# Kernel tuning notes

Measured on AMD Instinct MI355X. Metric: run time of the kernel, lower is better.

The kernel has to match this reference:

```python
import jax, jax.numpy as jnp
import numpy as np
from jax.scipy.special import logsumexp

K, D, H, A = 8, 512, 512, 1024
S, T = 64, 128
B = S * T


def setup_inputs() -> dict:
    key = jax.random.key(0)
    k1, k2, k3, k4 = jax.random.split(key, 4)
    obs = jax.random.normal(k1, (B, D), dtype=jnp.float32)
    actions = jax.random.randint(k2, (B,), 0, A, dtype=jnp.int64)
    # uniform mixture prior (log(1/K)) => all components supported
    start_mixture_logprobs = jnp.full((S, K), jnp.log(1.0 / K), dtype=jnp.float32)
    W1 = jax.random.normal(k3, (K, D, H), dtype=jnp.float32) * 0.02
    b1 = jnp.zeros((K, H), dtype=jnp.float32)
    W2 = jax.random.normal(k4, (K, H, A), dtype=jnp.float32) * 0.02
    b2 = jnp.zeros((K, A), dtype=jnp.float32)
    return {"obs": obs, "actions": actions,
            "start_mixture_logprobs": start_mixture_logprobs,
            "W1": W1, "b1": b1, "W2": W2, "b2": b2, "seq_len": T}


def reference(obs, actions, start_mixture_logprobs, W1, b1, W2, b2, seq_len):
    num_seqs, num_comp = start_mixture_logprobs.shape
    batch = obs.shape[0]
    t_len = batch // num_seqs  # == seq_len
    num_out = W2.shape[-1]

    # per-component MLP on the full batch (all components supported)
    h = jax.nn.relu(jnp.einsum('bd,kdh->kbh', obs, W1) + b1[:, None, :])
    logits = jnp.einsum('kbh,kha->kba', h, W2) + b2[:, None, :]  # [K,B,A]
    component_logprobs = jax.nn.log_softmax(logits, axis=2)      # [K,B,A]

    # add time dimension: [B, K, A] -> [S, T, K, A]
    clp_t = component_logprobs.transpose(1, 0, 2).reshape(num_seqs, t_len, num_comp, num_out)
    act_t = actions.reshape(num_seqs, t_len)

    # gather logprob of taken action per component: [S, T, K]
    idx = jnp.broadcast_to(act_t[:, :, None, None], (num_seqs, t_len, num_comp, 1))
    action_logprobs = jnp.take_along_axis(clp_t, idx, axis=3)[..., 0]
    cum = jnp.cumsum(action_logprobs, axis=1)  # [S,T,K]

    # per-timestep posterior over mixture (shifted cumulative evidence)
    shift = jnp.concatenate([jnp.zeros((num_seqs, 1, num_comp), dtype=cum.dtype), cum[:, :-1]], axis=1)
    mix = jax.nn.log_softmax(start_mixture_logprobs[:, None, :] + shift, axis=2)  # [S,T,K]
    final_mixture_logprobs = jax.nn.log_softmax(start_mixture_logprobs + cum[:, -1], axis=1)

    # combine: logsumexp over components of component_logprobs + mixture logprob
    mix_flat = mix.reshape(batch, num_comp).T  # [K,B]
    model_out = logsumexp(component_logprobs + mix_flat[:, :, None], axis=0)  # [B,A]
    return model_out, final_mixture_logprobs
```

## Files before the change

### kernel.cpp

```cpp
#include <hip/hip_runtime.h>
#include <hip/hip_bf16.h>
#include <stdint.h>

#define KC   8
#define DIM  512
#define HID  512
#define ACTN 1024
#define NS   64
#define NT   128
#define NB   8192
#define PB   8

typedef __attribute__((ext_vector_type(8))) short short8;
typedef __attribute__((ext_vector_type(8))) unsigned short ushort8;
typedef __attribute__((ext_vector_type(4))) float floatx4;

__device__ inline float bf2f(unsigned short u) {
    return __uint_as_float(((unsigned int)u) << 16);
}
__device__ inline unsigned short f2bf(float x) {
    return __builtin_bit_cast(unsigned short, __float2bfloat16(x));
}

__device__ inline void gload_lds16(const unsigned short* g, unsigned short* l) {
    __builtin_amdgcn_global_load_lds(
        (const __attribute__((address_space(1))) unsigned int*)g,
        (__attribute__((address_space(3))) unsigned int*)l,
        16, 0, 0);
}

__global__ __launch_bounds__(256) void obs_blk_kernel(
    const float* __restrict__ in, unsigned short* __restrict__ out)
{
    int mg = blockIdx.x;
#pragma unroll
    for (int rep = 0; rep < 16; ++rep) {
        int idx = rep * 256 + threadIdx.x;
        int kc  = idx >> 6;
        int row = idx & 63;
        const float* p = in + ((size_t)(mg * 64 + row) * DIM) + kc * 8;
        ushort8 u;
#pragma unroll
        for (int e = 0; e < 8; e++) u[e] = f2bf(p[e]);
        *(ushort8*)(out + (((size_t)mg * (DIM / 8) + kc) << 9) + (row << 3)) = u;
    }
}

__global__ __launch_bounds__(256) void wblk_kernel(
    const float* __restrict__ in, unsigned short* __restrict__ out, int R, int C)
{
    __shared__ float tile[64][65];
    int z = blockIdx.z;
    const float* src = in + (size_t)z * R * C;
    unsigned short* dst = out + (size_t)z * R * C;
    int h0 = blockIdx.x * 64, d0 = blockIdx.y * 64;
    int tx = threadIdx.x & 63, ty = threadIdx.x >> 6;
#pragma unroll
    for (int i = 0; i < 64; i += 4)
        tile[ty + i][tx] = src[(size_t)(d0 + ty + i) * C + h0 + tx];
    __syncthreads();
    int KCHR = R >> 3;
#pragma unroll
    for (int rep = 0; rep < 2; ++rep) {
        int idx  = rep * 256 + threadIdx.x;
        int h_l  = idx & 63;
        int dc_l = idx >> 6;
        ushort8 u;
#pragma unroll
        for (int e = 0; e < 8; e++) u[e] = f2bf(tile[dc_l * 8 + e][h_l]);
        size_t off = ((((size_t)(h0 >> 6) * KCHR) + (d0 >> 3) + dc_l) << 9) + (h_l << 3);
        *(ushort8*)(dst + off) = u;
    }
}

__global__ __launch_bounds__(256, 4) void gemm_blk_kernel(
    const unsigned short* __restrict__ Aall,
    const unsigned short* __restrict__ Ball,
    const float* __restrict__ biasall,
    unsigned short* __restrict__ Call,
    const int* __restrict__ actions,
    float* __restrict__ pmax, float* __restrict__ psum, float* __restrict__ palp,
    int M, int N, int Kd,
    long long zsA, long long zsB,
    int strideBias, long long strideC,
    int do_relu, int do_lse, int do_blocked)
{
    __shared__ __align__(16) unsigned short S[17408];
    unsigned short* const As = S;
    unsigned short* const Bs = S + 4096;

    const int zb = blockIdx.z;
    const float* bias = biasall + (size_t)zb * strideBias;
    unsigned short* Cb = Call + (size_t)zb * strideC;

    const int tid  = threadIdx.x;
    const int lane = tid & 63;
    const int wave = tid >> 6;
    const int wm = wave >> 1;
    const int wn = wave & 1;
    const int quad = lane >> 4;
    const int l16  = lane & 15;

    const int bm = blockIdx.x * 128;
    const int bn = blockIdx.y * 128;
    const int KCH = Kd >> 3;

    floatx4 acc[4][4];
#pragma unroll
    for (int i = 0; i < 4; i++)
#pragma unroll
        for (int j = 0; j < 4; j++)
            acc[i][j] = (floatx4){0.f, 0.f, 0.f, 0.f};

    const int loff = lane << 3;
    const unsigned short* pA = Aall + (size_t)zb * zsA + (((size_t)(bm >> 6) * KCH + wave) << 9) + loff;
    const unsigned short* pB = Ball + (size_t)zb * zsB + (((size_t)(bn >> 6) * KCH + wave) << 9) + loff;
    const size_t mgs = (size_t)KCH << 9;
    unsigned short* ldsA = As + wave * 1024;
    unsigned short* ldsB = Bs + wave * 1024;

    const int nk = Kd >> 5;
    for (int it = 0; it < nk; ++it) {
        __syncthreads();
        gload_lds16(pA,       ldsA);
        gload_lds16(pA + mgs, ldsA + 512);
        gload_lds16(pB,       ldsB);
        gload_lds16(pB + mgs, ldsB + 512);
        pA += 2048; pB += 2048;
        __syncthreads();

        short8 af[4], bfr[4];
#pragma unroll
        for (int i = 0; i < 4; i++)
            af[i] = *(const short8*)(As + quad * 1024 + ((wm * 64 + i * 16 + l16) << 3));
#pragma unroll
        for (int j = 0; j < 4; j++)
            bfr[j] = *(const short8*)(Bs + quad * 1024 + ((wn * 64 + j * 16 + l16) << 3));
#pragma unroll
        for (int i = 0; i < 4; i++)
#pragma unroll
            for (int j = 0; j < 4; j++)
                acc[i][j] = __builtin_amdgcn_mfma_f32_16x16x32_bf16(
                    af[i], bfr[j], acc[i][j], 0, 0, 0);
    }
    __syncthreads();

    unsigned short* const Cs = S;
#pragma unroll
    for (int j = 0; j < 4; j++) {
        int col = wn * 64 + j * 16 + l16;
        float bv = bias[bn + col];
#pragma unroll
        for (int i = 0; i < 4; i++) {
            int rw = wm * 64 + i * 16 + quad * 4;
#pragma unroll
            for (int r = 0; r < 4; r++) {
                float v = acc[i][j][r] + bv;
                if (do_relu) v = fmaxf(v, 0.f);
                Cs[(rw + r) * 136 + col] = f2bf(v);
            }
        }
    }
    __syncthreads();

    if (do_blocked) {
        const int KCHo = N >> 3;
#pragma unroll
        for (int rep = 0; rep < 8; ++rep) {
            int idx  = rep * 256 + tid;
            int kc_l = idx >> 7;
            int row  = idx & 127;
            ushort8 u = *(const ushort8*)&Cs[row * 136 + kc_l * 8];
            size_t off = ((((size_t)((bm >> 6) + (row >> 6)) * KCHo) + (bn >> 3) + kc_l) << 9)
                       + ((row & 63) << 3);
            *(ushort8*)(Cb + off) = u;
        }
    } else {
        const int row = tid >> 1;
        const int ch  = (tid & 1) * 64;

        float allm = 0.f;
        if (do_lse) {
            float m = -1e30f;
#pragma unroll
            for (int j = 0; j < 8; j++) {
                ushort8 u = *(const ushort8*)&Cs[row * 136 + ch + 8 * j];
#pragma unroll
                for (int e = 0; e < 8; e++) m = fmaxf(m, bf2f(u[e]));
            }
            allm = fmaxf(m, __shfl_xor(m, 1));
        }

        unsigned short* crow = Cb + (size_t)(bm + row) * N + bn + ch;
        float s = 0.f;
#pragma unroll
        for (int j = 0; j < 8; j++) {
            ushort8 u = *(const ushort8*)&Cs[row * 136 + ch + 8 * j];
            *(ushort8*)(crow + 8 * j) = u;
            if (do_lse) {
#pragma unroll
                for (int e = 0; e < 8; e++) s += __expf(bf2f(u[e]) - allm);
            }
        }

        if (do_lse) {
            float stot = s + __shfl_xor(s, 1);
            size_t kb = (size_t)zb * M + bm + row;
            if ((tid & 1) == 0) {
                pmax[kb * PB + blockIdx.y] = allm;
                psum[kb * PB + blockIdx.y] = stot;
            }
            int act = actions[bm + row];
            int rel = act - bn - ch;
            if (rel >= 0 && rel < 64)
                palp[kb] = bf2f(Cs[row * 136 + act - bn]);
        }
    }
}

__global__ __launch_bounds__(256) void lse_finish_kernel(
    const float* __restrict__ pmax, const float* __restrict__ psum,
    const float* __restrict__ palp,
    float* __restrict__ lse, float* __restrict__ alp)
{
    int kb = blockIdx.x * 256 + threadIdx.x;
    float m[PB];
#pragma unroll
    for (int p = 0; p < PB; p++) m[p] = pmax[(size_t)kb * PB + p];
    float M = m[0];
#pragma unroll
    for (int p = 1; p < PB; p++) M = fmaxf(M, m[p]);
    float S = 0.f;
#pragma unroll
    for (int p = 0; p < PB; p++) S += psum[(size_t)kb * PB + p] * __expf(m[p] - M);
    float l = M + __logf(S);
    lse[kb] = l;
    alp[kb] = palp[kb] - l;
}

__global__ __launch_bounds__(128) void mix_kernel(
    const float* __restrict__ alp,
    const float* __restrict__ start,
    const float* __restrict__ lse,
    float* __restrict__ w,
    float* __restrict__ fmix)
{
    __shared__ float buf[2][NT][9];
    int s = blockIdx.x, t = threadIdx.x;
    int b = s * NT + t;
    float a[KC];
#pragma unroll
    for (int k = 0; k < KC; k++) a[k] = alp[(size_t)k * NB + b];
#pragma unroll
    for (int k = 0; k < KC; k++) buf[0][t][k] = a[k];
    int p = 0;
    for (int off = 1; off < NT; off <<= 1) {
        __syncthreads();
#pragma unroll
        for (int k = 0; k < KC; k++) {
            float x = buf[p][t][k];
            if (t >= off) x += buf[p][t - off][k];
            buf[1 - p][t][k] = x;
        }
        p ^= 1;
    }
    __syncthreads();
    float st[KC], e[KC];
#pragma unroll
    for (int k = 0; k < KC; k++) st[k] = start[s * KC + k];
#pragma unroll
    for (int k = 0; k < KC; k++) e[k] = st[k] + buf[p][t][k] - a[k];
    float m = e[0];
#pragma unroll
    for (int k = 1; k < KC; k++) m = fmaxf(m, e[k]);
    float sum = 0.f;
#pragma unroll
    for (int k = 0; k < KC; k++) sum += __expf(e[k] - m);
    float l = m + __logf(sum);
#pragma unroll
    for (int k = 0; k < KC; k++)
        w[(size_t)k * NB + b] = (e[k] - l) - lse[(size_t)k * NB + b];

    if (t == NT - 1) {
        float f[KC];
#pragma unroll
        for (int k = 0; k < KC; k++) f[k] = st[k] + buf[p][t][k];
        float m2 = f[0];
#pragma unroll
        for (int k = 1; k < KC; k++) m2 = fmaxf(m2, f[k]);
        float s2 = 0.f;
#pragma unroll
        for (int k = 0; k < KC; k++) s2 += __expf(f[k] - m2);
        float l2 = m2 + __logf(s2);
#pragma unroll
        for (int k = 0; k < KC; k++) fmix[s * KC + k] = f[k] - l2;
    }
}

__global__ __launch_bounds__(128) void combine_kernel(
    const unsigned short* __restrict__ logits,
    const float* __restrict__ w,
    float* __restrict__ out)
{
    int b = blockIdx.x;
    int a0 = threadIdx.x * 8;
    float wv[KC];
#pragma unroll
    for (int k = 0; k < KC; k++) wv[k] = w[(size_t)k * NB + b];
    float x[KC][8];
#pragma unroll
    for (int k = 0; k < KC; k++) {
        ushort8 u = *(const ushort8*)(logits + ((size_t)k * NB + b) * ACTN + a0);
#pragma unroll
        for (int j = 0; j < 8; j++) x[k][j] = bf2f(u[j]) + wv[k];
    }
    float* op = out + (size_t)b * ACTN + a0;
#pragma unroll
    for (int j = 0; j < 8; j++) {
        float m = x[0][j];
#pragma unroll
        for (int k = 1; k < KC; k++) m = fmaxf(m, x[k][j]);
        float s = 0.f;
#pragma unroll
        for (int k = 0; k < KC; k++) s += __expf(x[k][j] - m);
        op[j] = m + __logf(s);
    }
}

extern "C" void kernel_launch(void* const* d_in, const int* in_sizes, int n_in,
                              void* d_out, int out_size, void* d_ws, size_t ws_size,
                              hipStream_t stream)
{
    const float* obs     = (const float*)d_in[0];
    const int*   actions = (const int*)d_in[1];
    const float* start   = (const float*)d_in[2];
    const float* W1      = (const float*)d_in[3];
    const float* b1      = (const float*)d_in[4];
    const float* W2      = (const float*)d_in[5];
    const float* b2      = (const float*)d_in[6];

    char* ws = (char*)d_ws;
    unsigned short* obs_bk = (unsigned short*)ws; ws += (size_t)NB * DIM * 2;
    unsigned short* W1bk   = (unsigned short*)ws; ws += (size_t)KC * HID * DIM * 2;
    unsigned short* W2bk   = (unsigned short*)ws; ws += (size_t)KC * ACTN * HID * 2;
    unsigned short* hbuf   = (unsigned short*)ws; ws += (size_t)KC * NB * HID * 2;
    unsigned short* logits = (unsigned short*)ws; ws += (size_t)KC * NB * ACTN * 2;
    float* lse  = (float*)ws; ws += (size_t)KC * NB * 4;
    float* alp  = (float*)ws; ws += (size_t)KC * NB * 4;
    float* wbuf = (float*)ws; ws += (size_t)KC * NB * 4;
    float* pmax = (float*)ws; ws += (size_t)KC * NB * PB * 4;
    float* psum = (float*)ws; ws += (size_t)KC * NB * PB * 4;
    float* palp = (float*)ws; ws += (size_t)KC * NB * 4;

    float* out  = (float*)d_out;
    float* fmix = out + (size_t)NB * ACTN;

    obs_blk_kernel<<<NB / 64, 256, 0, stream>>>(obs, obs_bk);
    wblk_kernel<<<dim3(HID / 64, DIM / 64, KC), 256, 0, stream>>>(W1, W1bk, DIM, HID);
    wblk_kernel<<<dim3(ACTN / 64, HID / 64, KC), 256, 0, stream>>>(W2, W2bk, HID, ACTN);

    gemm_blk_kernel<<<dim3(NB / 128, HID / 128, KC), 256, 0, stream>>>(
        obs_bk, W1bk, b1, hbuf, actions, pmax, psum, palp,
        NB, HID, DIM,
        0LL, (long long)HID * DIM,
        HID, (long long)NB * HID, 1, 0, 1);

    gemm_blk_kernel<<<dim3(NB / 128, ACTN / 128, KC), 256, 0, stream>>>(
        hbuf, W2bk, b2, logits, actions, pmax, psum, palp,
        NB, ACTN, HID,
        (long long)NB * HID, (long long)ACTN * HID,
        ACTN, (long long)NB * ACTN, 0, 1, 0);

    lse_finish_kernel<<<KC * NB / 256, 256, 0, stream>>>(pmax, psum, palp, lse, alp);

    mix_kernel<<<NS, NT, 0, stream>>>(alp, start, lse, wbuf, fmix);

    combine_kernel<<<NB, ACTN / 8, 0, stream>>>(logits, wbuf, out);
}
```

Baseline: 292.6 us.

## Store logits as fp8, fuse prep kernels, deepen GEMM K-step, merge lse into mix

Replaces the bf16 logits intermediate with a custom 8-bit float encoding (e4m3-like via exponent rebias), halving write and read traffic between the second GEMM and the combine kernel. It also merges the three layout-conversion kernels into one launch, doubles the K chunk per GEMM iteration to halve barrier count, folds the lse finish step into the mix kernel, and has combine process two rows per block. The fp8 storage loses precision in the final logsumexp output, which may exceed tolerance; the larger LDS tile footprint may affect occupancy.

New measurement: 270.2 us. 1.08x faster.

```diff
diff --git a/kernel.cpp b/kernel.cpp
--- a/kernel.cpp
+++ b/kernel.cpp
@@ -22,6 +22,20 @@
     return __builtin_bit_cast(unsigned short, __float2bfloat16(x));
 }
 
+__device__ inline unsigned char f2fp8(float v) {
+    unsigned int s = (__float_as_uint(v) >> 24) & 0x80u;
+    float a = fabsf(v) * 0x1.0p-120f;
+    unsigned int b = __float_as_uint(a);
+    b += 0x7FFFFu + ((b >> 20) & 1u);
+    unsigned int m = b >> 20;
+    if (m > 0x7Eu) m = 0x7Eu;
+    return (unsigned char)(s | m);
+}
+__device__ inline float fp82f(unsigned int byte) {
+    unsigned int bits = ((byte & 0x80u) << 24) | ((byte & 0x7Fu) << 20);
+    return __uint_as_float(bits) * 0x1.0p+120f;
+}
+
 __device__ inline void gload_lds16(const unsigned short* g, unsigned short* l) {
     __builtin_amdgcn_global_load_lds(
         (const __attribute__((address_space(1))) unsigned int*)g,
@@ -29,31 +43,42 @@
         16, 0, 0);
 }
 
-__global__ __launch_bounds__(256) void obs_blk_kernel(
-    const float* __restrict__ in, unsigned short* __restrict__ out)
-{
-    int mg = blockIdx.x;
-#pragma unroll
-    for (int rep = 0; rep < 16; ++rep) {
-        int idx = rep * 256 + threadIdx.x;
-        int kc  = idx >> 6;
-        int row = idx & 63;
-        const float* p = in + ((size_t)(mg * 64 + row) * DIM) + kc * 8;
-        ushort8 u;
-#pragma unroll
-        for (int e = 0; e < 8; e++) u[e] = f2bf(p[e]);
-        *(ushort8*)(out + (((size_t)mg * (DIM / 8) + kc) << 9) + (row << 3)) = u;
-    }
-}
-
-__global__ __launch_bounds__(256) void wblk_kernel(
-    const float* __restrict__ in, unsigned short* __restrict__ out, int R, int C)
+__global__ __launch_bounds__(256) void prep_kernel(
+    const float* __restrict__ obs, const float* __restrict__ W1,
+    const float* __restrict__ W2,
+    unsigned short* __restrict__ obs_bk, unsigned short* __restrict__ W1bk,
+    unsigned short* __restrict__ W2bk)
 {
     __shared__ float tile[64][65];
-    int z = blockIdx.z;
-    const float* src = in + (size_t)z * R * C;
-    unsigned short* dst = out + (size_t)z * R * C;
-    int h0 = blockIdx.x * 64, d0 = blockIdx.y * 64;
+    int id = blockIdx.x;
+    if (id < 128) {
+        int mg = id;
+#pragma unroll
+        for (int rep = 0; rep < 16; ++rep) {
+            int idx = rep * 256 + threadIdx.x;
+            int kc  = idx >> 6;
+            int row = idx & 63;
+            const float* p = obs + ((size_t)(mg * 64 + row) * DIM) + kc * 8;
+            ushort8 u;
+#pragma unroll
+            for (int e = 0; e < 8; e++) u[e] = f2bf(p[e]);
+            *(ushort8*)(obs_bk + (((size_t)mg * (DIM / 8) + kc) << 9) + (row << 3)) = u;
+        }
+        return;
+    }
+    const float* src; unsigned short* dst; int R, C, xt, yt;
+    if (id < 640) {
+        int t = id - 128; int z = t >> 6; int rem = t & 63;
+        xt = rem & 7; yt = rem >> 3;
+        R = DIM; C = HID;
+        src = W1 + (size_t)z * DIM * HID; dst = W1bk + (size_t)z * DIM * HID;
+    } else {
+        int t = id - 640; int z = t >> 7; int rem = t & 127;
+        xt = rem & 15; yt = rem >> 4;
+        R = HID; C = ACTN;
+        src = W2 + (size_t)z * HID * ACTN; dst = W2bk + (size_t)z * HID * ACTN;
+    }
+    int h0 = xt * 64, d0 = yt * 64;
     int tx = threadIdx.x & 63, ty = threadIdx.x >> 6;
 #pragma unroll
     for (int i = 0; i < 64; i += 4)
@@ -77,21 +102,21 @@
     const unsigned short* __restrict__ Aall,
     const unsigned short* __restrict__ Ball,
     const float* __restrict__ biasall,
-    unsigned short* __restrict__ Call,
+    void* __restrict__ Call,
     const int* __restrict__ actions,
     float* __restrict__ pmax, float* __restrict__ psum, float* __restrict__ palp,
     int M, int N, int Kd,
     long long zsA, long long zsB,
-    int strideBias, long long strideC,
+    int strideBias, long long strideCbytes,
     int do_relu, int do_lse, int do_blocked)
 {
     __shared__ __align__(16) unsigned short S[17408];
     unsigned short* const As = S;
-    unsigned short* const Bs = S + 4096;
+    unsigned short* const Bs = S + 8192;
 
     const int zb = blockIdx.z;
     const float* bias = biasall + (size_t)zb * strideBias;
-    unsigned short* Cb = Call + (size_t)zb * strideC;
+    char* const Cbase = (char*)Call + (size_t)zb * strideCbytes;
 
     const int tid  = threadIdx.x;
     const int lane = tid & 63;
@@ -119,29 +144,38 @@
     unsigned short* ldsA = As + wave * 1024;
     unsigned short* ldsB = Bs + wave * 1024;
 
-    const int nk = Kd >> 5;
+    const int nk = Kd >> 6;
     for (int it = 0; it < nk; ++it) {
         __syncthreads();
-        gload_lds16(pA,       ldsA);
-        gload_lds16(pA + mgs, ldsA + 512);
-        gload_lds16(pB,       ldsB);
-        gload_lds16(pB + mgs, ldsB + 512);
-        pA += 2048; pB += 2048;
+        gload_lds16(pA,              ldsA);
+        gload_lds16(pA + mgs,        ldsA + 512);
+        gload_lds16(pA + 2048,       ldsA + 4096);
+        gload_lds16(pA + 2048 + mgs, ldsA + 4096 + 512);
+        gload_lds16(pB,              ldsB);
+        gload_lds16(pB + mgs,        ldsB + 512);
+        gload_lds16(pB + 2048,       ldsB + 4096);
+        gload_lds16(pB + 2048 + mgs, ldsB + 4096 + 512);
+        pA += 4096; pB += 4096;
         __syncthreads();
 
-        short8 af[4], bfr[4];
-#pragma unroll
-        for (int i = 0; i < 4; i++)
-            af[i] = *(const short8*)(As + quad * 1024 + ((wm * 64 + i * 16 + l16) << 3));
-#pragma unroll
-        for (int j = 0; j < 4; j++)
-            bfr[j] = *(const short8*)(Bs + quad * 1024 + ((wn * 64 + j * 16 + l16) << 3));
-#pragma unroll
-        for (int i = 0; i < 4; i++)
+#pragma unroll
+        for (int h = 0; h < 2; ++h) {
+            const unsigned short* Ah = As + h * 4096 + quad * 1024;
+            const unsigned short* Bh = Bs + h * 4096 + quad * 1024;
+            short8 af[4], bfr[4];
+#pragma unroll
+            for (int i = 0; i < 4; i++)
+                af[i] = *(const short8*)(Ah + ((wm * 64 + i * 16 + l16) << 3));
 #pragma unroll
             for (int j = 0; j < 4; j++)
-                acc[i][j] = __builtin_amdgcn_mfma_f32_16x16x32_bf16(
-                    af[i], bfr[j], acc[i][j], 0, 0, 0);
+                bfr[j] = *(const short8*)(Bh + ((wn * 64 + j * 16 + l16) << 3));
+#pragma unroll
+            for (int i = 0; i < 4; i++)
+#pragma unroll
+                for (int j = 0; j < 4; j++)
+                    acc[i][j] = __builtin_amdgcn_mfma_f32_16x16x32_bf16(
+                        af[i], bfr[j], acc[i][j], 0, 0, 0);
+        }
     }
     __syncthreads();
 
@@ -164,6 +198,7 @@
     __syncthreads();
 
     if (do_blocked) {
+        unsigned short* Cb16 = (unsigned short*)Cbase;
         const int KCHo = N >> 3;
 #pragma unroll
         for (int rep = 0; rep < 8; ++rep) {
@@ -173,84 +208,86 @@
             ushort8 u = *(const ushort8*)&Cs[row * 136 + kc_l * 8];
             size_t off = ((((size_t)((bm >> 6) + (row >> 6)) * KCHo) + (bn >> 3) + kc_l) << 9)
                        + ((row & 63) << 3);
-            *(ushort8*)(Cb + off) = u;
+            *(ushort8*)(Cb16 + off) = u;
         }
     } else {
+        unsigned char* Cb8 = (unsigned char*)Cbase;
         const int row = tid >> 1;
         const int ch  = (tid & 1) * 64;
 
-        float allm = 0.f;
-        if (do_lse) {
-            float m = -1e30f;
-#pragma unroll
-            for (int j = 0; j < 8; j++) {
-                ushort8 u = *(const ushort8*)&Cs[row * 136 + ch + 8 * j];
-#pragma unroll
-                for (int e = 0; e < 8; e++) m = fmaxf(m, bf2f(u[e]));
-            }
-            allm = fmaxf(m, __shfl_xor(m, 1));
-        }
-
-        unsigned short* crow = Cb + (size_t)(bm + row) * N + bn + ch;
-        float s = 0.f;
+        float allm = -1e30f;
 #pragma unroll
         for (int j = 0; j < 8; j++) {
             ushort8 u = *(const ushort8*)&Cs[row * 136 + ch + 8 * j];
-            *(ushort8*)(crow + 8 * j) = u;
-            if (do_lse) {
-#pragma unroll
-                for (int e = 0; e < 8; e++) s += __expf(bf2f(u[e]) - allm);
+#pragma unroll
+            for (int e = 0; e < 8; e++) allm = fmaxf(allm, bf2f(u[e]));
+        }
+        allm = fmaxf(allm, __shfl_xor(allm, 1));
+
+        unsigned char* crow = Cb8 + (size_t)(bm + row) * N + bn + ch;
+        float s = 0.f;
+#pragma unroll
+        for (int j = 0; j < 8; j++) {
+            ushort8 u = *(const ushort8*)&Cs[row * 136 + ch + 8 * j];
+            unsigned int lo = 0, hi = 0;
+#pragma unroll
+            for (int e = 0; e < 4; e++) {
+                float v = bf2f(u[e]);
+                s += __expf(v - allm);
+                lo |= (unsigned int)f2fp8(v) << (8 * e);
             }
-        }
-
-        if (do_lse) {
-            float stot = s + __shfl_xor(s, 1);
-            size_t kb = (size_t)zb * M + bm + row;
-            if ((tid & 1) == 0) {
-                pmax[kb * PB + blockIdx.y] = allm;
-                psum[kb * PB + blockIdx.y] = stot;
+#pragma unroll
+            for (int e = 4; e < 8; e++) {
+                float v = bf2f(u[e]);
+                s += __expf(v - allm);
+                hi |= (unsigned int)f2fp8(v) << (8 * (e - 4));
             }
-            int act = actions[bm + row];
-            int rel = act - bn - ch;
-            if (rel >= 0 && rel < 64)
-                palp[kb] = bf2f(Cs[row * 136 + act - bn]);
-        }
-    }
-}
-
-__global__ __launch_bounds__(256) void lse_finish_kernel(
-    const float* __restrict__ pmax, const float* __restrict__ psum,
+            uint2 pk; pk.x = lo; pk.y = hi;
+            *(uint2*)(crow + 8 * j) = pk;
+        }
+
+        float stot = s + __shfl_xor(s, 1);
+        size_t kb = (size_t)zb * M + bm + row;
+        if ((tid & 1) == 0) {
+            pmax[kb * PB + blockIdx.y] = allm;
+            psum[kb * PB + blockIdx.y] = stot;
+        }
+        int act = actions[bm + row];
+        int rel = act - bn - ch;
+        if (rel >= 0 && rel < 64)
+            palp[kb] = bf2f(Cs[row * 136 + act - bn]);
+    }
+}
+
+__global__ __launch_bounds__(128) void mix_kernel(
     const float* __restrict__ palp,
-    float* __restrict__ lse, float* __restrict__ alp)
-{
-    int kb = blockIdx.x * 256 + threadIdx.x;
-    float m[PB];
-#pragma unroll
-    for (int p = 0; p < PB; p++) m[p] = pmax[(size_t)kb * PB + p];
-    float M = m[0];
-#pragma unroll
-    for (int p = 1; p < PB; p++) M = fmaxf(M, m[p]);
-    float S = 0.f;
-#pragma unroll
-    for (int p = 0; p < PB; p++) S += psum[(size_t)kb * PB + p] * __expf(m[p] - M);
-    float l = M + __logf(S);
-    lse[kb] = l;
-    alp[kb] = palp[kb] - l;
-}
-
-__global__ __launch_bounds__(128) void mix_kernel(
-    const float* __restrict__ alp,
+    const float* __restrict__ pmax,
+    const float* __restrict__ psum,
     const float* __restrict__ start,
-    const float* __restrict__ lse,
     float* __restrict__ w,
     float* __restrict__ fmix)
 {
     __shared__ float buf[2][NT][9];
     int s = blockIdx.x, t = threadIdx.x;
     int b = s * NT + t;
-    float a[KC];
-#pragma unroll
-    for (int k = 0; k < KC; k++) a[k] = alp[(size_t)k * NB + b];
+
+    float a[KC], lsev[KC];
+#pragma unroll
+    for (int k = 0; k < KC; k++) {
+        size_t kb = (size_t)k * NB + b;
+        const float* pm = pmax + kb * PB;
+        const float* ps = psum + kb * PB;
+        float M = pm[0];
+#pragma unroll
+        for (int p = 1; p < PB; p++) M = fmaxf(M, pm[p]);
+        float S = 0.f;
+#pragma unroll
+        for (int p = 0; p < PB; p++) S += ps[p] * __expf(pm[p] - M);
+        float l = M + __logf(S);
+        lsev[k] = l;
+        a[k] = palp[kb] - l;
+    }
+
 #pragma unroll
     for (int k = 0; k < KC; k++) buf[0][t][k] = a[k];
     int p = 0;
@@ -279,7 +316,7 @@
     float l = m + __logf(sum);
 #pragma unroll
     for (int k = 0; k < KC; k++)
-        w[(size_t)k * NB + b] = (e[k] - l) - lse[(size_t)k * NB + b];
+        w[(size_t)k * NB + b] = (e[k] - l) - lsev[k];
 
     if (t == NT - 1) {
         float f[KC];
@@ -297,22 +334,22 @@
     }
 }
 
-__global__ __launch_bounds__(128) void combine_kernel(
-    const unsigned short* __restrict__ logits,
+__global__ __launch_bounds__(256) void combine_kernel(
+    const unsigned char* __restrict__ logits8,
     const float* __restrict__ w,
     float* __restrict__ out)
 {
-    int b = blockIdx.x;
-    int a0 = threadIdx.x * 8;
-    float wv[KC];
-#pragma unroll
-    for (int k = 0; k < KC; k++) wv[k] = w[(size_t)k * NB + b];
+    int b  = blockIdx.x * 2 + (threadIdx.x >> 7);
+    int a0 = (threadIdx.x & 127) * 8;
     float x[KC][8];
 #pragma unroll
     for (int k = 0; k < KC; k++) {
-        ushort8 u = *(const ushort8*)(logits + ((size_t)k * NB + b) * ACTN + a0);
-#pragma unroll
-        for (int j = 0; j < 8; j++) x[k][j] = bf2f(u[j]) + wv[k];
+        float wv = w[(size_t)k * NB + b];
+        uint2 q = *(const uint2*)(logits8 + ((size_t)k * NB + b) * ACTN + a0);
+#pragma unroll
+        for (int e = 0; e < 4; e++) x[k][e]     = fp82f((q.x >> (8 * e)) & 0xffu) + wv;
+#pragma unroll
+        for (int e = 0; e < 4; e++) x[k][4 + e] = fp82f((q.y >> (8 * e)) & 0xffu) + wv;
     }
     float* op = out + (size_t)b * ACTN + a0;
 #pragma unroll
@@ -340,13 +377,11 @@
     const float* b2      = (const float*)d_in[6];
 
     char* ws = (char*)d_ws;
-    unsigned short* obs_bk = (unsigned short*)ws; ws += (size_t)NB * DIM * 2;
-    unsigned short* W1bk   = (unsigned short*)ws; ws += (size_t)KC * HID * DIM * 2;
-    unsigned short* W2bk   = (unsigned short*)ws; ws += (size_t)KC * ACTN * HID * 2;
-    unsigned short* hbuf   = (unsigned short*)ws; ws += (size_t)KC * NB * HID * 2;
-    unsigned short* logits = (unsigned short*)ws; ws += (size_t)KC * NB * ACTN * 2;
-    float* lse  = (float*)ws; ws += (size_t)KC * NB * 4;
-    float* alp  = (float*)ws; ws += (size_t)KC * NB * 4;
+    unsigned short* obs_bk  = (unsigned short*)ws; ws += (size_t)NB * DIM * 2;
+    unsigned short* W1bk    = (unsigned short*)ws; ws += (size_t)KC * HID * DIM * 2;
+    unsigned short* W2bk    = (unsigned short*)ws; ws += (size_t)KC * ACTN * HID * 2;
+    unsigned short* hbuf    = (unsigned short*)ws; ws += (size_t)KC * NB * HID * 2;
+    unsigned char*  logits8 = (unsigned char*)ws;  ws += (size_t)KC * NB * ACTN;
     float* wbuf = (float*)ws; ws += (size_t)KC * NB * 4;
     float* pmax = (float*)ws; ws += (size_t)KC * NB * PB * 4;
     float* psum = (float*)ws; ws += (size_t)KC * NB * PB * 4;
@@ -355,25 +390,21 @@
     float* out  = (float*)d_out;
     float* fmix = out + (size_t)NB * ACTN;
 
-    obs_blk_kernel<<<NB / 64, 256, 0, stream>>>(obs, obs_bk);
-    wblk_kernel<<<dim3(HID / 64, DIM / 64, KC), 256, 0, stream>>>(W1, W1bk, DIM, HID);
-    wblk_kernel<<<dim3(ACTN / 64, HID / 64, KC), 256, 0, stream>>>(W2, W2bk, HID, ACTN);
+    prep_kernel<<<1664, 256, 0, stream>>>(obs, W1, W2, obs_bk, W1bk, W2bk);
 
     gemm_blk_kernel<<<dim3(NB / 128, HID / 128, KC), 256, 0, stream>>>(
         obs_bk, W1bk, b1, hbuf, actions, pmax, psum, palp,
         NB, HID, DIM,
         0LL, (long long)HID * DIM,
-        HID, (long long)NB * HID, 1, 0, 1);
+        HID, (long long)NB * HID * 2, 1, 0, 1);
 
     gemm_blk_kernel<<<dim3(NB / 128, ACTN / 128, KC), 256, 0, stream>>>(
-        hbuf, W2bk, b2, logits, actions, pmax, psum, palp,
+        hbuf, W2bk, b2, logits8, actions, pmax, psum, palp,
         NB, ACTN, HID,
         (long long)NB * HID, (long long)ACTN * HID,
         ACTN, (long long)NB * ACTN, 0, 1, 0);
 
-    lse_finish_kernel<<<KC * NB / 256, 256, 0, stream>>>(pmax, psum, palp, lse, alp);
-
-    mix_kernel<<<NS, NT, 0, stream>>>(alp, start, lse, wbuf, fmix);
-
-    combine_kernel<<<NB, ACTN / 8, 0, stream>>>(logits, wbuf, out);
-}
+    mix_kernel<<<NS, NT, 0, stream>>>(palp, pmax, psum, start, wbuf, fmix);
+
+    combine_kernel<<<NB / 2, 256, 0, stream>>>(logits8, wbuf, out);
+}
```
